# Kernel optimization log

Hardware: AMD Instinct MI355X
Metric: run time of the kernel (lower is better)

Reference implementation:

```python
import jax, jax.numpy as jnp
import numpy as np

B, S, V, D, P, H = 64, 512, 30522, 768, 8, 4
DH = D // H            # per-head dim = 192
NPER = 1 + P           # 1 text node + P concept nodes per example
N = B * NPER           # 576 total GNN nodes
E = 4096               # raw edges (before symmetrization)
EPS = 1e-6
NEG_SLOPE = 0.2


def gat_layer(x, src_i, dst_i, W, a_s, a_d, b):
    """Standard multi-head GAT layer (concat heads), edge-list formulation."""
    n = x.shape[0]
    h = (x @ W).reshape(n, H, DH)                      # [N,H,DH]
    alpha_s = jnp.einsum('nhd,hd->nh', h, a_s)          # [N,H]
    alpha_d = jnp.einsum('nhd,hd->nh', h, a_d)
    e = jax.nn.leaky_relu(alpha_s[src_i] + alpha_d[dst_i], NEG_SLOPE)  # [E,H]
    m = jax.ops.segment_max(e, dst_i, num_segments=n)   # stable softmax per dst
    ex = jnp.exp(e - m[dst_i])
    den = jax.ops.segment_sum(ex, dst_i, num_segments=n)
    att = ex / den[dst_i]                               # [E,H]
    msg = att[:, :, None] * h[src_i]                    # [E,H,DH]
    out = jax.ops.segment_sum(msg, dst_i, num_segments=n)
    return out.reshape(n, D) + b


def setup_inputs() -> dict:
    key = jax.random.key(0)
    ks = jax.random.split(key, 14)
    src = jax.random.randint(ks[0], (B, S), 0, V)
    seg = jax.random.randint(ks[1], (B, S), 0, 3)
    type_ids = jax.random.randint(ks[2], (B, S), 0, 21)
    pos = jnp.broadcast_to(jnp.arange(S, dtype=jnp.int64 if jax.config.jax_enable_x64 else jnp.int32), (B, S))
    span_start = jax.random.randint(ks[3], (B, P), 0, S - 8)
    span_len = jax.random.randint(ks[4], (B, P), 1, 8)
    span_end = span_start + span_len                    # end >= start, < S
    edge_idx = jax.random.randint(ks[5], (2, E), 0, N)
    word_table = jax.random.normal(ks[6], (V, D), dtype=jnp.float32) * 0.02
    pos_table = jax.random.normal(ks[7], (S, D), dtype=jnp.float32) * 0.02
    seg_table = jax.random.normal(ks[8], (3, D), dtype=jnp.float32) * 0.02
    type_table = jax.random.normal(ks[9], (21, D), dtype=jnp.float32) * 0.02
    gamma = jnp.ones((D,), jnp.float32)
    beta = jnp.zeros((D,), jnp.float32)
    W_gat = jax.random.normal(ks[10], (5, D, D), dtype=jnp.float32) * 0.05
    a_src = jax.random.normal(ks[11], (5, H, DH), dtype=jnp.float32) * 0.05
    a_dst = jax.random.normal(ks[12], (5, H, DH), dtype=jnp.float32) * 0.05
    b_gat = jnp.zeros((5, D), jnp.float32)
    return dict(src=src, seg=seg, type_ids=type_ids, pos=pos,
                span_start=span_start, span_end=span_end, edge_idx=edge_idx,
                word_table=word_table, pos_table=pos_table, seg_table=seg_table,
                type_table=type_table, gamma=gamma, beta=beta,
                W_gat=W_gat, a_src=a_src, a_dst=a_dst, b_gat=b_gat)


def reference(src, seg, type_ids, pos, span_start, span_end, edge_idx,
              word_table, pos_table, seg_table, type_table, gamma, beta,
              W_gat, a_src, a_dst, b_gat):
    word_emb = word_table[src]                                  # [B,S,D]
    # --- GNN node assembly: node 0 = CLS emb, nodes 1..P = span sums ---
    pref = jnp.concatenate([jnp.zeros((B, 1, D), word_emb.dtype),
                            jnp.cumsum(word_emb, axis=1)], axis=1)  # [B,S+1,D]
    g = lambda idx: jnp.take_along_axis(pref, idx[:, :, None], axis=1)
    concept = g(span_end + 1) - g(span_start)                   # [B,P,D] inclusive span sums
    nodes = jnp.concatenate([word_emb[:, :1, :], concept], axis=1).reshape(N, D)
    # --- symmetrize edges (code concatenates flipped copy); add self-loops ---
    loop = jnp.arange(N)
    si = jnp.concatenate([edge_idx[0], edge_idx[1], loop])
    di = jnp.concatenate([edge_idx[1], edge_idx[0], loop])
    # --- 5 GAT layers with GELU (dropout = identity at eval) ---
    x = nodes
    for l in range(5):
        x = jax.nn.gelu(gat_layer(x, si, di, W_gat[l], a_src[l], a_dst[l], b_gat[l]),
                        approximate=False)
    text_idx = jnp.arange(B) * NPER
    word_emb = word_emb.at[:, 0, :].set(x[text_idx])            # scatter back into CLS slot
    # --- sum of 4 embeddings + LayerNorm ---
    emb = word_emb + pos_table[pos] + seg_table[seg] + type_table[type_ids]
    mu = jnp.mean(emb, axis=-1, keepdims=True)
    var = jnp.mean((emb - mu) ** 2, axis=-1, keepdims=True)
    return gamma * (emb - mu) / jnp.sqrt(var + EPS) + beta
```

## Files before the change

kernel.cpp:

```cpp
#include <hip/hip_runtime.h>


#define DEV __device__ __forceinline__

typedef short s16x8 __attribute__((ext_vector_type(8)));
typedef float f32x4 __attribute__((ext_vector_type(4)));
typedef unsigned short u16x8 __attribute__((ext_vector_type(8)));

DEV float b2f(unsigned int u) { union { unsigned int i; float f; } v; v.i = u << 16; return v.f; }
DEV unsigned short f2b(float f) {
  union { float f; unsigned int i; } v; v.f = f;
  return (unsigned short)((v.i + 0x7fffu + ((v.i >> 16) & 1u)) >> 16);
}
DEV float gelu_exact(float x) { return 0.5f * x * (1.f + erff(x * 0.70710678118654752f)); }

DEV float ldf(const void* p, size_t i, int fF) {
  return fF ? ((const float*)p)[i] : b2f(((const unsigned short*)p)[i]);
}
DEV int ldi(const void* p, size_t i, int fI) {
  return fI ? ((const int*)p)[2 * i] : ((const int*)p)[i];
}

DEV size_t frag_off(int n, int d) {
  return ((((size_t)(n >> 4) * 24 + (size_t)(d >> 5)) * 64 +
           (((d >> 3) & 3) << 4) + (n & 15)) << 3) + (d & 7);
}

__global__ __launch_bounds__(256) void k_front(const void* __restrict__ src,
                                               const void* __restrict__ sst,
                                               const void* __restrict__ sen,
                                               const void* __restrict__ edge,
                                               const void* __restrict__ word,
                                               const void* __restrict__ pos,
                                               const void* __restrict__ aS,
                                               const void* __restrict__ aD,
                                               const void* __restrict__ Wg,
                                               unsigned short* __restrict__ xh,
                                               unsigned short* __restrict__ xl,
                                               unsigned short* __restrict__ Bh,
                                               unsigned short* __restrict__ Bl,
                                               int* __restrict__ csr_off,
                                               int* __restrict__ csr_src,
                                               int* __restrict__ flags) {
  __shared__ int sflags[2];
  __shared__ float tile[64][65];
  __shared__ float sA[768], sD[768];
  __shared__ int cnt[576], off[577], fill[576];
  int t = threadIdx.x, bid = blockIdx.x;
  if (t < 64) {
    const unsigned short* w16 = (const unsigned short*)word;
    int crazy = 0;
    for (int i = t; i < 512; i += 64) {
      unsigned int e = (w16[i] >> 7) & 0xffu;
      if (e >= 135u || (e >= 1u && e <= 100u)) crazy++;
    }
#pragma unroll
    for (int o = 32; o > 0; o >>= 1) crazy += __shfl_down(crazy, o);
    if (t == 0) {
      sflags[0] = (crazy >= 8) ? 1 : 0;
      sflags[1] = (((const int*)pos)[1] == 0) ? 1 : 0;
    }
  }
  __syncthreads();
  int fF = sflags[0], fI = sflags[1];
  if (bid == 0 && t == 0) { flags[0] = fF; flags[1] = fI; }

  if (bid < 780) {
    int layer = bid / 156, r = bid % 156, kt = r / 13, nt = r % 13;
    int k0 = kt * 64, n0 = nt * 64;
    if (nt < 12) {
#pragma unroll
      for (int i = 0; i < 16; ++i) {
        int e = t + 256 * i, rk = e >> 6, cn = e & 63;
        tile[rk][cn] = ldf(Wg, ((size_t)layer * 768 + k0 + rk) * 768 + n0 + cn, fF);
      }
    } else {
      for (int i = t; i < 768; i += 256) {
        sA[i] = ldf(aS, (size_t)layer * 768 + i, fF);
        sD[i] = ldf(aD, (size_t)layer * 768 + i, fF);
      }
#pragma unroll
      for (int i = 0; i < 16; ++i) {
        int e = t + 256 * i, rk = e >> 6, cn = e & 63;
        if (cn >= 8) tile[rk][cn] = 0.f;
      }
      __syncthreads();
      int wave = t >> 6, lane = t & 63;
      for (int rr = 0; rr < 16; ++rr) {
        int rk = wave * 16 + rr;
        size_t wbase = ((size_t)layer * 768 + k0 + rk) * 768;
        float accS[4] = {0.f, 0.f, 0.f, 0.f}, accD[4] = {0.f, 0.f, 0.f, 0.f};
#pragma unroll
        for (int i = 0; i < 12; ++i) {
          int d = lane + 64 * i;
          float w = ldf(Wg, wbase + d, fF);
          accS[i / 3] += w * sA[d];
          accD[i / 3] += w * sD[d];
        }
#pragma unroll
        for (int h = 0; h < 4; ++h) {
          float sS = accS[h], sDv = accD[h];
#pragma unroll
          for (int o = 32; o > 0; o >>= 1) {
            sS += __shfl_down(sS, o);
            sDv += __shfl_down(sDv, o);
          }
          if (lane == 0) { tile[rk][h] = sS; tile[rk][4 + h] = sDv; }
        }
      }
    }
    __syncthreads();
    size_t lb = (size_t)layer * 79872;
#pragma unroll
    for (int g = 0; g < 2; ++g) {
      int G = t * 2 + g, rn = G & 63, c8 = G >> 6;
      int n = n0 + rn, kb = k0 + c8 * 8;
      u16x8 hv, lv;
#pragma unroll
      for (int j = 0; j < 8; ++j) {
        float v = tile[c8 * 8 + j][rn];
        unsigned short hi = f2b(v);
        hv[j] = hi;
        lv[j] = f2b(v - b2f((unsigned int)hi));
      }
      size_t go = lb + ((size_t)(n >> 4) * 24 + (size_t)(kb >> 5)) * 64 +
                  (((kb >> 3) & 3) << 4) + (n & 15);
      *(u16x8*)(Bh + go * 8) = hv;
      *(u16x8*)(Bl + go * 8) = lv;
    }
  } else if (bid < 1356) {
    int g = bid - 780;
    int b = g / 9, j = g % 9;
    float v[3] = {0.f, 0.f, 0.f};
    if (j == 0) {
      int rr = ldi(src, (size_t)b * 512, fI);
#pragma unroll
      for (int ii = 0; ii < 3; ++ii) v[ii] = ldf(word, (size_t)rr * 768 + t + 256 * ii, fF);
    } else {
      int st = ldi(sst, (size_t)b * 8 + j - 1, fI);
      int en = ldi(sen, (size_t)b * 8 + j - 1, fI);
      for (int s = st; s <= en; ++s) {
        int rr = ldi(src, (size_t)b * 512 + s, fI);
#pragma unroll
        for (int ii = 0; ii < 3; ++ii) v[ii] += ldf(word, (size_t)rr * 768 + t + 256 * ii, fF);
      }
    }
#pragma unroll
    for (int ii = 0; ii < 3; ++ii) {
      int d = t + 256 * ii;
      unsigned short hi = f2b(v[ii]);
      size_t o = frag_off(g, d);
      xh[o] = hi;
      xl[o] = f2b(v[ii] - b2f((unsigned int)hi));
    }
  } else {
    for (int i = t; i < 576; i += 256) cnt[i] = 0;
    __syncthreads();
    for (int e = t; e < 8768; e += 256) {
      int di;
      if (e < 4096) di = ldi(edge, (size_t)4096 + e, fI);
      else if (e < 8192) di = ldi(edge, (size_t)e - 4096, fI);
      else di = e - 8192;
      atomicAdd(&cnt[di], 1);
    }
    __syncthreads();
    if (t == 0) {
      int a = 0;
      for (int i = 0; i < 576; ++i) { off[i] = a; a += cnt[i]; }
      off[576] = a;
    }
    __syncthreads();
    for (int i = t; i < 577; i += 256) csr_off[i] = off[i];
    for (int i = t; i < 576; i += 256) fill[i] = off[i];
    __syncthreads();
    for (int e = t; e < 8768; e += 256) {
      int si, di;
      if (e < 4096)      { si = ldi(edge, (size_t)e, fI); di = ldi(edge, (size_t)4096 + e, fI); }
      else if (e < 8192) { si = ldi(edge, (size_t)e, fI); di = ldi(edge, (size_t)e - 4096, fI); }
      else               { si = e - 8192;                 di = si; }
      int p = atomicAdd(&fill[di], 1);
      csr_src[p] = si;
    }
  }
}

__global__ __launch_bounds__(256) void k_gemm(const unsigned short* __restrict__ xh,
                                              const unsigned short* __restrict__ xl,
                                              const unsigned short* __restrict__ Bh,
                                              const unsigned short* __restrict__ Bl,
                                              float* __restrict__ C) {
  int t = threadIdx.x;
  int wid = blockIdx.x * 4 + (t >> 6), lane = t & 63;
  int rt = wid / 52, ct = wid % 52;
  const s16x8* Ah = (const s16x8*)xh + (size_t)rt * 1536 + lane;
  const s16x8* Al = (const s16x8*)xl + (size_t)rt * 1536 + lane;
  const s16x8* Bhp = (const s16x8*)Bh + (size_t)ct * 1536 + lane;
  const s16x8* Blp = (const s16x8*)Bl + (size_t)ct * 1536 + lane;
  f32x4 a0 = {0.f, 0.f, 0.f, 0.f}, a1 = a0, a2 = a0;
#pragma unroll 6
  for (int kk = 0; kk < 24; ++kk) {
    s16x8 ah = Ah[kk * 64];
    s16x8 al = Al[kk * 64];
    s16x8 bh = Bhp[kk * 64];
    s16x8 bl = Blp[kk * 64];
    a0 = __builtin_amdgcn_mfma_f32_16x16x32_bf16(ah, bh, a0, 0, 0, 0);
    a1 = __builtin_amdgcn_mfma_f32_16x16x32_bf16(ah, bl, a1, 0, 0, 0);
    a2 = __builtin_amdgcn_mfma_f32_16x16x32_bf16(al, bh, a2, 0, 0, 0);
  }
  int row0 = rt * 16 + (lane >> 4) * 4, col = ct * 16 + (lane & 15);
#pragma unroll
  for (int r = 0; r < 4; ++r)
    C[(size_t)(row0 + r) * 832 + col] = a0[r] + a1[r] + a2[r];
}

__global__ __launch_bounds__(256) void k_gat(const float* __restrict__ C,
                                             const int* __restrict__ off,
                                             const int* __restrict__ srcs,
                                             const void* __restrict__ bG,
                                             const int* __restrict__ flg,
                                             int layer,
                                             float* __restrict__ xf,
                                             unsigned short* __restrict__ xh,
                                             unsigned short* __restrict__ xl) {
  int fF = flg[0];
  int idx = blockIdx.x * 256 + threadIdx.x;
  int n = idx / 768, d = idx - n * 768, h = d / 192;
  float aDv = C[(size_t)n * 832 + 772 + h];
  int e0 = off[n], e1 = off[n + 1];
  float num = 0.f, den = 0.f;
  for (int e = e0; e < e1; ++e) {
    int s = srcs[e];
    float lg = C[(size_t)s * 832 + 768 + h] + aDv;
    float lrel = lg < 0.f ? 0.2f * lg : lg;
    lrel = fminf(fmaxf(lrel, -60.f), 40.f);
    float w = __expf(lrel);
    num += w * C[(size_t)s * 832 + d];
    den += w;
  }
  float g = gelu_exact(num / den + ldf(bG, (size_t)layer * 768 + d, fF));
  xf[idx] = g;
  unsigned short hi = f2b(g);
  size_t o = frag_off(n, d);
  xh[o] = hi;
  xl[o] = f2b(g - b2f((unsigned int)hi));
}

DEV void final_row_f32(int r, int lane, const f32x4* wsrc,
                       const void* seg, const void* typ, const void* post,
                       const void* segt, const void* typt,
                       const void* gamma, const void* beta, int fI,
                       float* __restrict__ outp) {
  int s = r & 511;
  int sg = ldi(seg, (size_t)r, fI), tp = ldi(typ, (size_t)r, fI);
  const f32x4* pr = (const f32x4*)((const float*)post + (size_t)s * 768);
  const f32x4* sr = (const f32x4*)((const float*)segt + (size_t)sg * 768);
  const f32x4* tr = (const f32x4*)((const float*)typt + (size_t)tp * 768);
  float sum = 0.f, sq = 0.f;
  f32x4 vv[3];
#pragma unroll
  for (int j = 0; j < 3; ++j) {
    int p = lane + 64 * j;
    f32x4 a = wsrc[j];
    a += pr[p]; a += sr[p]; a += tr[p];
    vv[j] = a;
#pragma unroll
    for (int c = 0; c < 4; ++c) { sum += a[c]; sq += a[c] * a[c]; }
  }
#pragma unroll
  for (int o = 32; o > 0; o >>= 1) { sum += __shfl_down(sum, o); sq += __shfl_down(sq, o); }
  sum = __shfl(sum, 0); sq = __shfl(sq, 0);
  float mu = sum * (1.f / 768.f);
  float var = fmaxf(sq * (1.f / 768.f) - mu * mu, 0.f);
  float rstd = rsqrtf(var + 1e-6f);
  const f32x4* gm = (const f32x4*)gamma;
  const f32x4* bt = (const f32x4*)beta;
  f32x4* orow = (f32x4*)(outp + (size_t)r * 768);
#pragma unroll
  for (int j = 0; j < 3; ++j) {
    int p = lane + 64 * j;
    f32x4 g4 = gm[p], b4 = bt[p], y;
#pragma unroll
    for (int c = 0; c < 4; ++c) y[c] = g4[c] * (vv[j][c] - mu) * rstd + b4[c];
    __builtin_nontemporal_store(y, &orow[p]);
  }
}

DEV void final_row_bf16(int r, int lane, const void* src, const void* seg,
                        const void* typ, const void* word, const void* post,
                        const void* segt, const void* typt, const void* gamma,
                        const void* beta, const float* xf, int fI,
                        unsigned short* __restrict__ outp) {
  int b = r >> 9, s = r & 511;
  int sg = ldi(seg, (size_t)r, fI), tp = ldi(typ, (size_t)r, fI);
  int wrow = ldi(src, (size_t)r, fI);
  bool cls = (s == 0);
  float sum = 0.f, sq = 0.f;
  float vs[12];
#pragma unroll
  for (int j = 0; j < 12; ++j) {
    int d = lane + 64 * j;
    float xv = cls ? xf[(size_t)b * 6912 + d] : ldf(word, (size_t)wrow * 768 + d, 0);
    xv += ldf(post, (size_t)s * 768 + d, 0);
    xv += ldf(segt, (size_t)sg * 768 + d, 0);
    xv += ldf(typt, (size_t)tp * 768 + d, 0);
    vs[j] = xv;
    sum += xv; sq += xv * xv;
  }
#pragma unroll
  for (int o = 32; o > 0; o >>= 1) { sum += __shfl_down(sum, o); sq += __shfl_down(sq, o); }
  sum = __shfl(sum, 0); sq = __shfl(sq, 0);
  float mu = sum * (1.f / 768.f);
  float var = fmaxf(sq * (1.f / 768.f) - mu * mu, 0.f);
  float rstd = rsqrtf(var + 1e-6f);
#pragma unroll
  for (int j = 0; j < 12; ++j) {
    int d = lane + 64 * j;
    float y = ldf(gamma, (size_t)d, 0) * (vs[j] - mu) * rstd + ldf(beta, (size_t)d, 0);
    outp[(size_t)r * 768 + d] = f2b(y);
  }
}

__global__ __launch_bounds__(256) void k_final(const void* __restrict__ src,
                                               const void* __restrict__ seg,
                                               const void* __restrict__ typ,
                                               const void* __restrict__ word,
                                               const void* __restrict__ post,
                                               const void* __restrict__ segt,
                                               const void* __restrict__ typt,
                                               const void* __restrict__ gamma,
                                               const void* __restrict__ beta,
                                               const float* __restrict__ xf,
                                               const int* __restrict__ flg,
                                               void* __restrict__ out) {
  int fF = flg[0], fI = flg[1];
  int wave = threadIdx.x >> 6, lane = threadIdx.x & 63;
  int r0 = blockIdx.x * 4 + wave, r1 = r0 + 16384;
  if (fF) {
    int s0 = r0 & 511, s1 = r1 & 511;
    int b0 = r0 >> 9, b1 = r1 >> 9;
    int w0r = ldi(src, (size_t)r0, fI), w1r = ldi(src, (size_t)r1, fI);
    const f32x4* p0 = (s0 == 0) ? (const f32x4*)(xf + (size_t)b0 * 6912)
                                : (const f32x4*)((const float*)word + (size_t)w0r * 768);
    const f32x4* p1 = (s1 == 0) ? (const f32x4*)(xf + (size_t)b1 * 6912)
                                : (const f32x4*)((const float*)word + (size_t)w1r * 768);
    f32x4 wa[3], wb[3];
#pragma unroll
    for (int j = 0; j < 3; ++j) { wa[j] = p0[lane + 64 * j]; wb[j] = p1[lane + 64 * j]; }
    final_row_f32(r0, lane, wa, seg, typ, post, segt, typt, gamma, beta, fI, (float*)out);
    final_row_f32(r1, lane, wb, seg, typ, post, segt, typt, gamma, beta, fI, (float*)out);
  } else {
    final_row_bf16(r0, lane, src, seg, typ, word, post, segt, typt, gamma, beta, xf, fI,
                   (unsigned short*)out);
    final_row_bf16(r1, lane, src, seg, typ, word, post, segt, typt, gamma, beta, xf, fI,
                   (unsigned short*)out);
  }
}

extern "C" void kernel_launch(void* const* d_in, const int* in_sizes, int n_in,
                              void* d_out, int out_size, void* d_ws, size_t ws_size,
                              hipStream_t stream) {
  const void* src  = d_in[0];
  const void* seg  = d_in[1];
  const void* typ  = d_in[2];
  const void* pos  = d_in[3];
  const void* sst  = d_in[4];
  const void* sen  = d_in[5];
  const void* edge = d_in[6];
  const void* word = d_in[7];
  const void* post = d_in[8];
  const void* segt = d_in[9];
  const void* typt = d_in[10];
  const void* gamma = d_in[11];
  const void* beta  = d_in[12];
  const void* Wg    = d_in[13];
  const void* aS    = d_in[14];
  const void* aD    = d_in[15];
  const void* bG    = d_in[16];

  char* ws = (char*)d_ws;
  float* xf = (float*)(ws);
  float* C  = (float*)(ws + 1769472);
  unsigned short* xh = (unsigned short*)(ws + 3686400);
  unsigned short* xl = (unsigned short*)(ws + 4571136);
  unsigned short* Bh = (unsigned short*)(ws + 5455872);
  unsigned short* Bl = (unsigned short*)(ws + 11845632);
  int* csr_off = (int*)(ws + 18358272);
  int* csr_src = (int*)(ws + 18360592);
  int* flags   = (int*)(ws + 18395664);

  k_front<<<dim3(1357), dim3(256), 0, stream>>>(src, sst, sen, edge, word, pos, aS, aD, Wg,
                                                xh, xl, Bh, Bl, csr_off, csr_src, flags);
  for (int l = 0; l < 5; ++l) {
    k_gemm<<<dim3(468), dim3(256), 0, stream>>>(xh, xl,
                                                Bh + (size_t)l * 832 * 768,
                                                Bl + (size_t)l * 832 * 768, C);
    k_gat<<<dim3(1728), dim3(256), 0, stream>>>(C, csr_off, csr_src, bG, flags, l, xf, xh, xl);
  }
  k_final<<<dim3(4096), dim3(256), 0, stream>>>(src, seg, typ, word, post, segt, typt,
                                                gamma, beta, xf, flags, d_out);
}
```

Before: 389.1 us.

## Overlap non-CLS embedding LayerNorm with first GAT GEMM; shrink GEMM blocks

The final embedding-sum plus LayerNorm for all non-CLS rows does not depend on the GNN, so it now runs inside the first GEMM launch as extra blocks, each wave handling four rows. A small kernel afterwards writes only the 64 CLS rows. Later GEMM launches use 64-thread blocks, one wave each, to spread work over more CUs. The aim is to hide the bandwidth-heavy output pass behind the serial GNN chain, at the cost of competing with the first GEMM for memory bandwidth.

```diff
diff --git a/kernel.cpp b/kernel.cpp
--- a/kernel.cpp
+++ b/kernel.cpp
@@ -184,13 +184,12 @@
   }
 }
 
-__global__ __launch_bounds__(256) void k_gemm(const unsigned short* __restrict__ xh,
-                                              const unsigned short* __restrict__ xl,
-                                              const unsigned short* __restrict__ Bh,
-                                              const unsigned short* __restrict__ Bl,
-                                              float* __restrict__ C) {
-  int t = threadIdx.x;
-  int wid = blockIdx.x * 4 + (t >> 6), lane = t & 63;
+DEV void gemm_wave(int wid, int lane,
+                   const unsigned short* __restrict__ xh,
+                   const unsigned short* __restrict__ xl,
+                   const unsigned short* __restrict__ Bh,
+                   const unsigned short* __restrict__ Bl,
+                   float* __restrict__ C) {
   int rt = wid / 52, ct = wid % 52;
   const s16x8* Ah = (const s16x8*)xh + (size_t)rt * 1536 + lane;
   const s16x8* Al = (const s16x8*)xl + (size_t)rt * 1536 + lane;
@@ -211,6 +210,143 @@
 #pragma unroll
   for (int r = 0; r < 4; ++r)
     C[(size_t)(row0 + r) * 832 + col] = a0[r] + a1[r] + a2[r];
+}
+
+__global__ __launch_bounds__(64) void k_gemm(const unsigned short* __restrict__ xh,
+                                             const unsigned short* __restrict__ xl,
+                                             const unsigned short* __restrict__ Bh,
+                                             const unsigned short* __restrict__ Bl,
+                                             float* __restrict__ C) {
+  gemm_wave(blockIdx.x, threadIdx.x & 63, xh, xl, Bh, Bl, C);
+}
+
+DEV void final_row_f32(int r, int lane, const f32x4* wsrc,
+                       const void* seg, const void* typ, const void* post,
+                       const void* segt, const void* typt,
+                       const void* gamma, const void* beta, int fI,
+                       float* __restrict__ outp) {
+  int s = r & 511;
+  int sg = ldi(seg, (size_t)r, fI), tp = ldi(typ, (size_t)r, fI);
+  const f32x4* pr = (const f32x4*)((const float*)post + (size_t)s * 768);
+  const f32x4* sr = (const f32x4*)((const float*)segt + (size_t)sg * 768);
+  const f32x4* tr = (const f32x4*)((const float*)typt + (size_t)tp * 768);
+  float sum = 0.f, sq = 0.f;
+  f32x4 vv[3];
+#pragma unroll
+  for (int j = 0; j < 3; ++j) {
+    int p = lane + 64 * j;
+    f32x4 a = wsrc[j];
+    a += pr[p]; a += sr[p]; a += tr[p];
+    vv[j] = a;
+#pragma unroll
+    for (int c = 0; c < 4; ++c) { sum += a[c]; sq += a[c] * a[c]; }
+  }
+#pragma unroll
+  for (int o = 32; o > 0; o >>= 1) { sum += __shfl_down(sum, o); sq += __shfl_down(sq, o); }
+  sum = __shfl(sum, 0); sq = __shfl(sq, 0);
+  float mu = sum * (1.f / 768.f);
+  float var = fmaxf(sq * (1.f / 768.f) - mu * mu, 0.f);
+  float rstd = rsqrtf(var + 1e-6f);
+  const f32x4* gm = (const f32x4*)gamma;
+  const f32x4* bt = (const f32x4*)beta;
+  f32x4* orow = (f32x4*)(outp + (size_t)r * 768);
+#pragma unroll
+  for (int j = 0; j < 3; ++j) {
+    int p = lane + 64 * j;
+    f32x4 g4 = gm[p], b4 = bt[p], y;
+#pragma unroll
+    for (int c = 0; c < 4; ++c) y[c] = g4[c] * (vv[j][c] - mu) * rstd + b4[c];
+    __builtin_nontemporal_store(y, &orow[p]);
+  }
+}
+
+DEV void final_row_bf16(int r, int lane, const void* src, const void* seg,
+                        const void* typ, const void* word, const void* post,
+                        const void* segt, const void* typt, const void* gamma,
+                        const void* beta, const float* xf, int fI,
+                        unsigned short* __restrict__ outp) {
+  int b = r >> 9, s = r & 511;
+  int sg = ldi(seg, (size_t)r, fI), tp = ldi(typ, (size_t)r, fI);
+  int wrow = ldi(src, (size_t)r, fI);
+  bool cls = (s == 0);
+  float sum = 0.f, sq = 0.f;
+  float vs[12];
+#pragma unroll
+  for (int j = 0; j < 12; ++j) {
+    int d = lane + 64 * j;
+    float xv = cls ? xf[(size_t)b * 6912 + d] : ldf(word, (size_t)wrow * 768 + d, 0);
+    xv += ldf(post, (size_t)s * 768 + d, 0);
+    xv += ldf(segt, (size_t)sg * 768 + d, 0);
+    xv += ldf(typt, (size_t)tp * 768 + d, 0);
+    vs[j] = xv;
+    sum += xv; sq += xv * xv;
+  }
+#pragma unroll
+  for (int o = 32; o > 0; o >>= 1) { sum += __shfl_down(sum, o); sq += __shfl_down(sq, o); }
+  sum = __shfl(sum, 0); sq = __shfl(sq, 0);
+  float mu = sum * (1.f / 768.f);
+  float var = fmaxf(sq * (1.f / 768.f) - mu * mu, 0.f);
+  float rstd = rsqrtf(var + 1e-6f);
+#pragma unroll
+  for (int j = 0; j < 12; ++j) {
+    int d = lane + 64 * j;
+    float y = ldf(gamma, (size_t)d, 0) * (vs[j] - mu) * rstd + ldf(beta, (size_t)d, 0);
+    outp[(size_t)r * 768 + d] = f2b(y);
+  }
+}
+
+__global__ __launch_bounds__(256) void k_gemm0f(const unsigned short* __restrict__ xh,
+                                                const unsigned short* __restrict__ xl,
+                                                const unsigned short* __restrict__ Bh,
+                                                const unsigned short* __restrict__ Bl,
+                                                float* __restrict__ C,
+                                                const void* __restrict__ src,
+                                                const void* __restrict__ seg,
+                                                const void* __restrict__ typ,
+                                                const void* __restrict__ word,
+                                                const void* __restrict__ post,
+                                                const void* __restrict__ segt,
+                                                const void* __restrict__ typt,
+                                                const void* __restrict__ gamma,
+                                                const void* __restrict__ beta,
+                                                const int* __restrict__ flg,
+                                                void* __restrict__ out) {
+  int t = threadIdx.x, wave = t >> 6, lane = t & 63;
+  if (blockIdx.x < 468) {
+    gemm_wave(blockIdx.x * 4 + wave, lane, xh, xl, Bh, Bl, C);
+    return;
+  }
+  int fF = flg[0], fI = flg[1];
+  int wv = (blockIdx.x - 468) * 4 + wave;
+  int rr[4];
+#pragma unroll
+  for (int k = 0; k < 4; ++k) {
+    int rid = wv + 8176 * k;
+    int b = rid / 511, s = 1 + (rid - b * 511);
+    rr[k] = b * 512 + s;
+  }
+  if (fF) {
+    const f32x4* wp[4];
+#pragma unroll
+    for (int k = 0; k < 4; ++k) {
+      int w = ldi(src, (size_t)rr[k], fI);
+      wp[k] = (const f32x4*)((const float*)word + (size_t)w * 768);
+    }
+    f32x4 wa[4][3];
+#pragma unroll
+    for (int k = 0; k < 4; ++k)
+#pragma unroll
+      for (int j = 0; j < 3; ++j) wa[k][j] = wp[k][lane + 64 * j];
+#pragma unroll
+    for (int k = 0; k < 4; ++k)
+      final_row_f32(rr[k], lane, wa[k], seg, typ, post, segt, typt, gamma, beta, fI,
+                    (float*)out);
+  } else {
+#pragma unroll
+    for (int k = 0; k < 4; ++k)
+      final_row_bf16(rr[k], lane, src, seg, typ, word, post, segt, typt, gamma, beta,
+                     (const float*)nullptr, fI, (unsigned short*)out);
+  }
 }
 
 __global__ __launch_bounds__(256) void k_gat(const float* __restrict__ C,
@@ -245,113 +381,30 @@
   xl[o] = f2b(g - b2f((unsigned int)hi));
 }
 
-DEV void final_row_f32(int r, int lane, const f32x4* wsrc,
-                       const void* seg, const void* typ, const void* post,
-                       const void* segt, const void* typt,
-                       const void* gamma, const void* beta, int fI,
-                       float* __restrict__ outp) {
-  int s = r & 511;
-  int sg = ldi(seg, (size_t)r, fI), tp = ldi(typ, (size_t)r, fI);
-  const f32x4* pr = (const f32x4*)((const float*)post + (size_t)s * 768);
-  const f32x4* sr = (const f32x4*)((const float*)segt + (size_t)sg * 768);
-  const f32x4* tr = (const f32x4*)((const float*)typt + (size_t)tp * 768);
-  float sum = 0.f, sq = 0.f;
-  f32x4 vv[3];
-#pragma unroll
-  for (int j = 0; j < 3; ++j) {
-    int p = lane + 64 * j;
-    f32x4 a = wsrc[j];
-    a += pr[p]; a += sr[p]; a += tr[p];
-    vv[j] = a;
-#pragma unroll
-    for (int c = 0; c < 4; ++c) { sum += a[c]; sq += a[c] * a[c]; }
-  }
-#pragma unroll
-  for (int o = 32; o > 0; o >>= 1) { sum += __shfl_down(sum, o); sq += __shfl_down(sq, o); }
-  sum = __shfl(sum, 0); sq = __shfl(sq, 0);
-  float mu = sum * (1.f / 768.f);
-  float var = fmaxf(sq * (1.f / 768.f) - mu * mu, 0.f);
-  float rstd = rsqrtf(var + 1e-6f);
-  const f32x4* gm = (const f32x4*)gamma;
-  const f32x4* bt = (const f32x4*)beta;
-  f32x4* orow = (f32x4*)(outp + (size_t)r * 768);
-#pragma unroll
-  for (int j = 0; j < 3; ++j) {
-    int p = lane + 64 * j;
-    f32x4 g4 = gm[p], b4 = bt[p], y;
-#pragma unroll
-    for (int c = 0; c < 4; ++c) y[c] = g4[c] * (vv[j][c] - mu) * rstd + b4[c];
-    __builtin_nontemporal_store(y, &orow[p]);
-  }
-}
-
-DEV void final_row_bf16(int r, int lane, const void* src, const void* seg,
-                        const void* typ, const void* word, const void* post,
-                        const void* segt, const void* typt, const void* gamma,
-                        const void* beta, const float* xf, int fI,
-                        unsigned short* __restrict__ outp) {
-  int b = r >> 9, s = r & 511;
-  int sg = ldi(seg, (size_t)r, fI), tp = ldi(typ, (size_t)r, fI);
-  int wrow = ldi(src, (size_t)r, fI);
-  bool cls = (s == 0);
-  float sum = 0.f, sq = 0.f;
-  float vs[12];
-#pragma unroll
-  for (int j = 0; j < 12; ++j) {
-    int d = lane + 64 * j;
-    float xv = cls ? xf[(size_t)b * 6912 + d] : ldf(word, (size_t)wrow * 768 + d, 0);
-    xv += ldf(post, (size_t)s * 768 + d, 0);
-    xv += ldf(segt, (size_t)sg * 768 + d, 0);
-    xv += ldf(typt, (size_t)tp * 768 + d, 0);
-    vs[j] = xv;
-    sum += xv; sq += xv * xv;
-  }
-#pragma unroll
-  for (int o = 32; o > 0; o >>= 1) { sum += __shfl_down(sum, o); sq += __shfl_down(sq, o); }
-  sum = __shfl(sum, 0); sq = __shfl(sq, 0);
-  float mu = sum * (1.f / 768.f);
-  float var = fmaxf(sq * (1.f / 768.f) - mu * mu, 0.f);
-  float rstd = rsqrtf(var + 1e-6f);
-#pragma unroll
-  for (int j = 0; j < 12; ++j) {
-    int d = lane + 64 * j;
-    float y = ldf(gamma, (size_t)d, 0) * (vs[j] - mu) * rstd + ldf(beta, (size_t)d, 0);
-    outp[(size_t)r * 768 + d] = f2b(y);
-  }
-}
-
-__global__ __launch_bounds__(256) void k_final(const void* __restrict__ src,
-                                               const void* __restrict__ seg,
-                                               const void* __restrict__ typ,
-                                               const void* __restrict__ word,
-                                               const void* __restrict__ post,
-                                               const void* __restrict__ segt,
-                                               const void* __restrict__ typt,
-                                               const void* __restrict__ gamma,
-                                               const void* __restrict__ beta,
-                                               const float* __restrict__ xf,
-                                               const int* __restrict__ flg,
-                                               void* __restrict__ out) {
+__global__ __launch_bounds__(256) void k_final_cls(const void* __restrict__ src,
+                                                   const void* __restrict__ seg,
+                                                   const void* __restrict__ typ,
+                                                   const void* __restrict__ word,
+                                                   const void* __restrict__ post,
+                                                   const void* __restrict__ segt,
+                                                   const void* __restrict__ typt,
+                                                   const void* __restrict__ gamma,
+                                                   const void* __restrict__ beta,
+                                                   const float* __restrict__ xf,
+                                                   const int* __restrict__ flg,
+                                                   void* __restrict__ out) {
   int fF = flg[0], fI = flg[1];
   int wave = threadIdx.x >> 6, lane = threadIdx.x & 63;
-  int r0 = blockIdx.x * 4 + wave, r1 = r0 + 16384;
+  int b = blockIdx.x * 4 + wave;
+  int r = b * 512;
   if (fF) {
-    int s0 = r0 & 511, s1 = r1 & 511;
-    int b0 = r0 >> 9, b1 = r1 >> 9;
-    int w0r = ldi(src, (size_t)r0, fI), w1r = ldi(src, (size_t)r1, fI);
-    const f32x4* p0 = (s0 == 0) ? (const f32x4*)(xf + (size_t)b0 * 6912)
-                                : (const f32x4*)((const float*)word + (size_t)w0r * 768);
-    const f32x4* p1 = (s1 == 0) ? (const f32x4*)(xf + (size_t)b1 * 6912)
-                                : (const f32x4*)((const float*)word + (size_t)w1r * 768);
-    f32x4 wa[3], wb[3];
-#pragma unroll
-    for (int j = 0; j < 3; ++j) { wa[j] = p0[lane + 64 * j]; wb[j] = p1[lane + 64 * j]; }
-    final_row_f32(r0, lane, wa, seg, typ, post, segt, typt, gamma, beta, fI, (float*)out);
-    final_row_f32(r1, lane, wb, seg, typ, post, segt, typt, gamma, beta, fI, (float*)out);
+    const f32x4* xr = (const f32x4*)(xf + (size_t)b * 6912);
+    f32x4 wa[3];
+#pragma unroll
+    for (int j = 0; j < 3; ++j) wa[j] = xr[lane + 64 * j];
+    final_row_f32(r, lane, wa, seg, typ, post, segt, typt, gamma, beta, fI, (float*)out);
   } else {
-    final_row_bf16(r0, lane, src, seg, typ, word, post, segt, typt, gamma, beta, xf, fI,
-                   (unsigned short*)out);
-    final_row_bf16(r1, lane, src, seg, typ, word, post, segt, typt, gamma, beta, xf, fI,
+    final_row_bf16(r, lane, src, seg, typ, word, post, segt, typt, gamma, beta, xf, fI,
                    (unsigned short*)out);
   }
 }
@@ -390,12 +443,16 @@
 
   k_front<<<dim3(1357), dim3(256), 0, stream>>>(src, sst, sen, edge, word, pos, aS, aD, Wg,
                                                 xh, xl, Bh, Bl, csr_off, csr_src, flags);
-  for (int l = 0; l < 5; ++l) {
-    k_gemm<<<dim3(468), dim3(256), 0, stream>>>(xh, xl,
+  k_gemm0f<<<dim3(2512), dim3(256), 0, stream>>>(xh, xl, Bh, Bl, C,
+                                                 src, seg, typ, word, post, segt, typt,
+                                                 gamma, beta, flags, d_out);
+  k_gat<<<dim3(1728), dim3(256), 0, stream>>>(C, csr_off, csr_src, bG, flags, 0, xf, xh, xl);
+  for (int l = 1; l < 5; ++l) {
+    k_gemm<<<dim3(1872), dim3(64), 0, stream>>>(xh, xl,
                                                 Bh + (size_t)l * 832 * 768,
                                                 Bl + (size_t)l * 832 * 768, C);
     k_gat<<<dim3(1728), dim3(256), 0, stream>>>(C, csr_off, csr_src, bG, flags, l, xf, xh, xl);
   }
-  k_final<<<dim3(4096), dim3(256), 0, stream>>>(src, seg, typ, word, post, segt, typt,
-                                                gamma, beta, xf, flags, d_out);
-}
+  k_final_cls<<<dim3(16), dim3(256), 0, stream>>>(src, seg, typ, word, post, segt, typt,
+                                                  gamma, beta, xf, flags, d_out);
+}
```

Result: slower. 399.8 us (+2.7%).
